# Kernel optimization log

Hardware: AMD Instinct MI355X
Metric: run time of the kernel (lower is better)

Reference implementation:

```python
import jax, jax.numpy as jnp
import numpy as np

K = 9          # kernel_size
PAD = 4        # padding
N_OUT, C_IN = 32, 32


def setup_inputs() -> dict:
    key = jax.random.key(0)
    k1, k2, k3, k4, k5 = jax.random.split(key, 5)
    x = jax.random.normal(k1, (16, C_IN, 192, 192), jnp.float32)
    sx = jax.random.uniform(k2, (N_OUT, C_IN), jnp.float32, 0.2, 4.0)
    sy = jax.random.uniform(k3, (N_OUT, C_IN), jnp.float32, 0.2, 4.0)
    th = jax.random.uniform(k4, (N_OUT, C_IN), jnp.float32, 0.0, 2.0 * np.pi)
    weight = jnp.stack([sx, sy, th], axis=-1)          # [N, C, 3]
    bias = jax.random.normal(k5, (N_OUT,), jnp.float32) * 0.01
    return {"x": x, "weight": weight, "bias": bias}


def _gaussian_kernels(weight, k):
    # weight: [N, C, 3] -> normalized anisotropic Gaussian kernels [N, C, k, k]
    sx, sy = weight[..., 0], weight[..., 1]
    rad = weight[..., 2] / 180.0 * jnp.pi          # matches theta/180*pi in source
    c, s = jnp.cos(rad), jnp.sin(rad)
    sx2, sy2 = sx * sx, sy * sy
    # Sigma = U diag(sx^2, sy^2) U^T, U = [[c,-s],[s,c]] -> Sigma = [[a,b],[b,d]]
    a = c * c * sx2 + s * s * sy2
    b = c * s * (sx2 - sy2)
    d = s * s * sx2 + c * c * sy2
    det = a * d - b * b
    ia, ib, id_ = d / det, -b / det, a / det       # closed-form 2x2 inverse
    ax = jnp.arange(k, dtype=jnp.float32) - k // 2
    xx = ax[None, :]                               # x varies along columns
    yy = ax[:, None]                               # y varies along rows
    # quadratic form: ia*x^2 + 2*ib*x*y + id*y^2, broadcast to [N, C, k, k]
    q = (ia[..., None, None] * (xx * xx)
         + 2.0 * ib[..., None, None] * (xx * yy)
         + id_[..., None, None] * (yy * yy))
    ker = jnp.exp(-0.5 * q)
    return ker / jnp.sum(ker, axis=(-2, -1), keepdims=True)


def reference(x, weight, bias):
    w = _gaussian_kernels(weight, K)               # [N, C, K, K]
    out = jax.lax.conv_general_dilated(
        x, w, window_strides=(1, 1), padding=[(PAD, PAD), (PAD, PAD)],
        dimension_numbers=("NCHW", "OIHW", "NCHW"))
    return out + bias[None, :, None, None]
```

## Files before the change

### kernel.cpp

```cpp
#include <hip/hip_runtime.h>

#define H 192
#define W 192
#define CIN 32
#define NOUT 32
#define NB 16
#define PADI 4

#define HT 16
#define WTL 16
#define RROWS 24
#define RCOLS 24

typedef __attribute__((ext_vector_type(8))) short bf16x8;
typedef __attribute__((ext_vector_type(4))) float f32x4;

__device__ __forceinline__ unsigned short f2bf(float f) {
    union { float f; unsigned int u; } v; v.f = f;
    unsigned int r = v.u + 0x7fffu + ((v.u >> 16) & 1u);
    return (unsigned short)(r >> 16);
}

__global__ void genw_kernel(const float* __restrict__ wp, unsigned short* __restrict__ W2g) {
    const int b = blockIdx.x;
    const int o = b >> 5;
    const int i = b & 31;
    const int t = threadIdx.x;

    float sx = wp[b * 3 + 0], sy = wp[b * 3 + 1], th = wp[b * 3 + 2];
    float rad = th / 180.0f * 3.14159265358979323846f;
    float co = cosf(rad), si = sinf(rad);
    float sx2 = sx * sx, sy2 = sy * sy;
    float a = co * co * sx2 + si * si * sy2;
    float bb = co * si * (sx2 - sy2);
    float d = si * si * sx2 + co * co * sy2;
    float det = a * d - bb * bb;
    float ia = d / det, ib = -bb / det, idd = a / det;

    const int tap = t;
    float e = 0.0f;
    if (tap < 81) {
        float xx = (float)(tap % 9 - 4);
        float yy = (float)(tap / 9 - 4);
        float q = ia * xx * xx + 2.0f * ib * xx * yy + idd * yy * yy;
        e = expf(-0.5f * q);
    }
    float s = e;
    #pragma unroll
    for (int off = 32; off > 0; off >>= 1) s += __shfl_down(s, off);
    __shared__ float ws[2];
    if ((t & 63) == 0) ws[t >> 6] = s;
    __syncthreads();
    float total = ws[0] + ws[1];

    if (tap < 81) {
        int mt = o >> 4, m = o & 15, quad = i >> 3, j = i & 7;
        W2g[((((mt * 81 + tap) * 4 + quad) * 16 + m) << 3) + j] = f2bf(e / total);
    }
}

__global__ __launch_bounds__(256, 4) void conv_kernel(
    const float* __restrict__ x, const unsigned short* __restrict__ W2g,
    const float* __restrict__ bias, float* __restrict__ out)
{
    __shared__ __align__(16) unsigned short ldsx[4 * RROWS * RCOLS * 8];

    const int t = threadIdx.x;
    const int bid = (blockIdx.x & 7) * 288 + (blockIdx.x >> 3);
    const int wb = bid % (W / WTL);
    const int hb = (bid / (W / WTL)) % (H / HT);
    const int n  = bid / ((W / WTL) * (H / HT));
    const int row0 = hb * HT - PADI;
    const int col0 = wb * WTL - PADI;
    const float* xn = x + (size_t)n * CIN * H * W;

    float v[9][8];
    #pragma unroll
    for (int it = 0; it < 9; ++it) {
        int idx = it * 256 + t;
        int w = idx % RCOLS;
        int r = (idx / RCOLS) % RROWS;
        int quad = idx / (RCOLS * RROWS);
        int row = row0 + r, col = col0 + w;
        #pragma unroll
        for (int k = 0; k < 8; k++) v[it][k] = 0.0f;
        if ((unsigned)row < (unsigned)H && (unsigned)col < (unsigned)W) {
            const float* p = xn + ((size_t)(quad * 8) * H + row) * W + col;
            #pragma unroll
            for (int k = 0; k < 8; k++) v[it][k] = p[(size_t)k * H * W];
        }
    }
    #pragma unroll
    for (int it = 0; it < 9; ++it) {
        int idx = it * 256 + t;
        unsigned int d[4];
        #pragma unroll
        for (int k = 0; k < 4; k++)
            d[k] = (unsigned int)f2bf(v[it][2 * k]) | ((unsigned int)f2bf(v[it][2 * k + 1]) << 16);
        *(uint4*)&ldsx[(size_t)idx * 8] = make_uint4(d[0], d[1], d[2], d[3]);
    }

    const int wave = t >> 6;
    const int lane = t & 63;
    const int l15 = lane & 15;
    const int quad4 = lane >> 4;
    const int mt = wave & 1;
    const int rbase = (wave >> 1) * 8;

    const bf16x8* __restrict__ Wp = (const bf16x8*)W2g;

    bf16x8 A[2][9];
    #pragma unroll
    for (int dy = 0; dy < 9; dy++)
        A[0][dy] = Wp[((mt * 81 + dy * 9 + 0) * 4 + quad4) * 16 + l15];

    __syncthreads();

    f32x4 acc[8];
    #pragma unroll
    for (int i = 0; i < 8; i++) acc[i] = (f32x4){0.f, 0.f, 0.f, 0.f};

    const unsigned short* bptr = &ldsx[(size_t)(((quad4 * RROWS + rbase) * RCOLS) + l15) * 8];

    #pragma unroll
    for (int dx = 0; dx < 9; dx++) {
        const int cur = dx & 1, nxt = cur ^ 1;
        if (dx < 8) {
            #pragma unroll
            for (int dy = 0; dy < 9; dy++)
                A[nxt][dy] = Wp[((mt * 81 + dy * 9 + (dx + 1)) * 4 + quad4) * 16 + l15];
        }
        #pragma unroll
        for (int rr = 0; rr < 16; rr++) {
            const bf16x8 bfrag = *(const bf16x8*)&bptr[(size_t)(rr * RCOLS + dx) * 8];
            #pragma unroll
            for (int dy = 0; dy < 9; dy++) {
                const int orr = rr - dy;
                if (orr >= 0 && orr < 8) {
                    acc[orr] = __builtin_amdgcn_mfma_f32_16x16x32_bf16(
                        A[cur][dy], bfrag, acc[orr], 0, 0, 0);
                }
            }
        }
    }

    float* outn = out + (size_t)n * NOUT * H * W;
    float bb[4];
    #pragma unroll
    for (int reg = 0; reg < 4; reg++) bb[reg] = bias[mt * 16 + quad4 * 4 + reg];
    #pragma unroll
    for (int orr = 0; orr < 8; orr++) {
        const int row = hb * HT + rbase + orr;
        const int col = wb * WTL + l15;
        #pragma unroll
        for (int reg = 0; reg < 4; reg++) {
            const int och = mt * 16 + quad4 * 4 + reg;
            outn[((size_t)och * H + row) * W + col] = acc[orr][reg] + bb[reg];
        }
    }
}

extern "C" void kernel_launch(void* const* d_in, const int* in_sizes, int n_in,
                              void* d_out, int out_size, void* d_ws, size_t ws_size,
                              hipStream_t stream) {
    const float* x    = (const float*)d_in[0];
    const float* wp   = (const float*)d_in[1];
    const float* bias = (const float*)d_in[2];
    float* out = (float*)d_out;
    unsigned short* W2g = (unsigned short*)d_ws;

    genw_kernel<<<NOUT * CIN, 128, 0, stream>>>(wp, W2g);
    const int blocks = NB * (H / HT) * (W / WTL);
    conv_kernel<<<blocks, 256, 0, stream>>>(x, W2g, bias, out);
}
```

Baseline: 189.9 us.

## Pre-pad and convert input to bf16 layout, load tiles via global_load_lds

Adds a pre-pass kernel that writes the input as a zero-padded bf16 buffer, with 8 channels packed per pixel, into the workspace. The conv kernel then copies its halo tile straight into LDS with 16-byte global_load_lds transfers, so it no longer does strided fp32 gathers, bounds checks or conversion per block. It also raises wave priority around the MFMA loop. The cost is an extra kernel launch plus a full write and read of a roughly 41 MB intermediate, and the old path is kept as a fallback when the workspace is too small.

```diff
diff --git a/kernel.cpp b/kernel.cpp
--- a/kernel.cpp
+++ b/kernel.cpp
@@ -1,4 +1,5 @@
 #include <hip/hip_runtime.h>
+#include <stdint.h>
 
 #define H 192
 #define W 192
@@ -6,6 +7,8 @@
 #define NOUT 32
 #define NB 16
 #define PADI 4
+#define HP 200
+#define WP 200
 
 #define HT 16
 #define WTL 16
@@ -19,6 +22,12 @@
     union { float f; unsigned int u; } v; v.f = f;
     unsigned int r = v.u + 0x7fffu + ((v.u >> 16) & 1u);
     return (unsigned short)(r >> 16);
+}
+
+__device__ __forceinline__ void gload_lds16(const void* g, void* l) {
+    __builtin_amdgcn_global_load_lds(
+        (const __attribute__((address_space(1))) void*)g,
+        (__attribute__((address_space(3))) void*)l, 16, 0, 0);
 }
 
 __global__ void genw_kernel(const float* __restrict__ wp, unsigned short* __restrict__ W2g) {
@@ -59,7 +68,121 @@
     }
 }
 
+__global__ __launch_bounds__(256) void xpad_kernel(
+    const float* __restrict__ x, unsigned short* __restrict__ xb)
+{
+    const int gid = blockIdx.x * 256 + threadIdx.x;
+    const int wpix = gid % WP;
+    int rest = gid / WP;
+    const int rp = rest % HP;
+    rest /= HP;
+    const int quad = rest & 3;
+    const int n = rest >> 2;
+
+    const int row = rp - PADI;
+    const int col = wpix - PADI;
+
+    unsigned int d[4] = {0u, 0u, 0u, 0u};
+    if ((unsigned)row < (unsigned)H && (unsigned)col < (unsigned)W) {
+        const float* p = x + (((size_t)(n * CIN + quad * 8)) * H + row) * (size_t)W + col;
+        float v[8];
+        #pragma unroll
+        for (int k = 0; k < 8; k++) v[k] = p[(size_t)k * H * W];
+        #pragma unroll
+        for (int k = 0; k < 4; k++)
+            d[k] = (unsigned int)f2bf(v[2 * k]) | ((unsigned int)f2bf(v[2 * k + 1]) << 16);
+    }
+    *(uint4*)&xb[(size_t)gid * 8] = make_uint4(d[0], d[1], d[2], d[3]);
+}
+
 __global__ __launch_bounds__(256, 4) void conv_kernel(
+    const unsigned short* __restrict__ xb, const unsigned short* __restrict__ W2g,
+    const float* __restrict__ bias, float* __restrict__ out)
+{
+    __shared__ __align__(16) unsigned short ldsx[4 * RROWS * RCOLS * 8];
+
+    const int t = threadIdx.x;
+    const int bid = (blockIdx.x & 7) * 288 + (blockIdx.x >> 3);
+    const int wb = bid % (W / WTL);
+    const int hb = (bid / (W / WTL)) % (H / HT);
+    const int n  = bid / ((W / WTL) * (H / HT));
+    const int r0p = hb * HT;
+    const int c0p = wb * WTL;
+    const unsigned short* xbn = xb + (size_t)n * 4 * HP * WP * 8;
+
+    #pragma unroll
+    for (int it = 0; it < 9; ++it) {
+        const int idx = it * 256 + t;
+        const int w = idx % RCOLS;
+        const int r = (idx / RCOLS) % RROWS;
+        const int quad = idx / (RCOLS * RROWS);
+        const size_t goff = (((size_t)(quad * HP + r0p + r)) * WP + (c0p + w)) * 8;
+        gload_lds16(xbn + goff, &ldsx[(size_t)idx * 8]);
+    }
+
+    const int wave = t >> 6;
+    const int lane = t & 63;
+    const int l15 = lane & 15;
+    const int quad4 = lane >> 4;
+    const int mt = wave & 1;
+    const int rbase = (wave >> 1) * 8;
+
+    const bf16x8* __restrict__ Wpt = (const bf16x8*)W2g;
+
+    bf16x8 A[2][9];
+    #pragma unroll
+    for (int dy = 0; dy < 9; dy++)
+        A[0][dy] = Wpt[((mt * 81 + dy * 9 + 0) * 4 + quad4) * 16 + l15];
+
+    __syncthreads();
+
+    f32x4 acc[8];
+    #pragma unroll
+    for (int i = 0; i < 8; i++) acc[i] = (f32x4){0.f, 0.f, 0.f, 0.f};
+
+    const unsigned short* bptr = &ldsx[(size_t)(((quad4 * RROWS + rbase) * RCOLS) + l15) * 8];
+
+    #pragma unroll
+    for (int dx = 0; dx < 9; dx++) {
+        const int cur = dx & 1, nxt = cur ^ 1;
+        if (dx < 8) {
+            #pragma unroll
+            for (int dy = 0; dy < 9; dy++)
+                A[nxt][dy] = Wpt[((mt * 81 + dy * 9 + (dx + 1)) * 4 + quad4) * 16 + l15];
+        }
+        __builtin_amdgcn_s_setprio(1);
+        #pragma unroll
+        for (int rr = 0; rr < 16; rr++) {
+            const bf16x8 bfrag = *(const bf16x8*)&bptr[(size_t)(rr * RCOLS + dx) * 8];
+            #pragma unroll
+            for (int dy = 0; dy < 9; dy++) {
+                const int orr = rr - dy;
+                if (orr >= 0 && orr < 8) {
+                    acc[orr] = __builtin_amdgcn_mfma_f32_16x16x32_bf16(
+                        A[cur][dy], bfrag, acc[orr], 0, 0, 0);
+                }
+            }
+        }
+        __builtin_amdgcn_s_setprio(0);
+    }
+
+    float* outn = out + (size_t)n * NOUT * H * W;
+    float bb[4];
+    #pragma unroll
+    for (int reg = 0; reg < 4; reg++) bb[reg] = bias[mt * 16 + quad4 * 4 + reg];
+    #pragma unroll
+    for (int orr = 0; orr < 8; orr++) {
+        const int row = hb * HT + rbase + orr;
+        const int col = wb * WTL + l15;
+        #pragma unroll
+        for (int reg = 0; reg < 4; reg++) {
+            const int och = mt * 16 + quad4 * 4 + reg;
+            outn[((size_t)och * H + row) * W + col] = acc[orr][reg] + bb[reg];
+        }
+    }
+}
+
+__global__ __launch_bounds__(256, 4) void conv_kernel_legacy(
     const float* __restrict__ x, const unsigned short* __restrict__ W2g,
     const float* __restrict__ bias, float* __restrict__ out)
 {
@@ -107,12 +230,12 @@
     const int mt = wave & 1;
     const int rbase = (wave >> 1) * 8;
 
-    const bf16x8* __restrict__ Wp = (const bf16x8*)W2g;
+    const bf16x8* __restrict__ Wpt = (const bf16x8*)W2g;
 
     bf16x8 A[2][9];
     #pragma unroll
     for (int dy = 0; dy < 9; dy++)
-        A[0][dy] = Wp[((mt * 81 + dy * 9 + 0) * 4 + quad4) * 16 + l15];
+        A[0][dy] = Wpt[((mt * 81 + dy * 9 + 0) * 4 + quad4) * 16 + l15];
 
     __syncthreads();
 
@@ -128,7 +251,7 @@
         if (dx < 8) {
             #pragma unroll
             for (int dy = 0; dy < 9; dy++)
-                A[nxt][dy] = Wp[((mt * 81 + dy * 9 + (dx + 1)) * 4 + quad4) * 16 + l15];
+                A[nxt][dy] = Wpt[((mt * 81 + dy * 9 + (dx + 1)) * 4 + quad4) * 16 + l15];
         }
         #pragma unroll
         for (int rr = 0; rr < 16; rr++) {
@@ -167,9 +290,21 @@
     const float* wp   = (const float*)d_in[1];
     const float* bias = (const float*)d_in[2];
     float* out = (float*)d_out;
+
     unsigned short* W2g = (unsigned short*)d_ws;
+    const size_t XB_OFF = 262144;
+    const size_t XB_BYTES = (size_t)NB * 4 * HP * WP * 8 * 2;
+    unsigned short* xb = (unsigned short*)((char*)d_ws + XB_OFF);
 
     genw_kernel<<<NOUT * CIN, 128, 0, stream>>>(wp, W2g);
+
     const int blocks = NB * (H / HT) * (W / WTL);
-    conv_kernel<<<blocks, 256, 0, stream>>>(x, W2g, bias, out);
-}
+
+    if (ws_size >= XB_OFF + XB_BYTES) {
+        const int xpad_blocks = (NB * 4 * HP * WP) / 256;
+        xpad_kernel<<<xpad_blocks, 256, 0, stream>>>(x, xb);
+        conv_kernel<<<blocks, 256, 0, stream>>>(xb, W2g, bias, out);
+    } else {
+        conv_kernel_legacy<<<blocks, 256, 0, stream>>>(x, W2g, bias, out);
+    }
+}
```

Result: no change. 192.3 us (+1.3%).
